# Optimization experiments

Hardware: AMD Instinct MI355X
Metric: run time of the kernel (lower is better)

Reference implementation:

```python
import jax, jax.numpy as jnp
import numpy as np

NEG_INF = -1e9  # fp32-safe mask value for non-edges
ALPHA = 0.2     # LeakyReLU negative slope


def setup_inputs() -> dict:
    key = jax.random.key(0)
    k1, k2, k3, k4, k5 = jax.random.split(key, 5)
    N, F_in, H, F_out = 4096, 512, 8, 64
    features = jax.random.normal(k1, (N, F_in), dtype=jnp.float32)
    adjacency_matrix = jax.random.randint(k2, (N, N), 0, 2, dtype=jnp.int32)
    W = jax.random.normal(k3, (H, F_in, F_out), dtype=jnp.float32) * (F_in ** -0.5)
    a_src = jax.random.normal(k4, (H, F_out), dtype=jnp.float32) * (F_out ** -0.5)
    a_dst = jax.random.normal(k5, (H, F_out), dtype=jnp.float32) * (F_out ** -0.5)
    return {"features": features, "adjacency_matrix": adjacency_matrix,
            "W": W, "a_src": a_src, "a_dst": a_dst}


def reference(features, adjacency_matrix, W, a_src, a_dst):
    # Per-head linear projection: [H, N, F_out]
    Wh = jnp.einsum('nf,hfo->hno', features, W)
    # Attention logits e_ij = LeakyReLU(a_src . Wh_i + a_dst . Wh_j)
    src = jnp.einsum('hno,ho->hn', Wh, a_src)  # [H, N]
    dst = jnp.einsum('hno,ho->hn', Wh, a_dst)  # [H, N]
    e = jax.nn.leaky_relu(src[:, :, None] + dst[:, None, :], ALPHA)  # [H, N, N]
    mask = (adjacency_matrix > 0)[None, :, :]
    e = jnp.where(mask, e, jnp.asarray(NEG_INF, e.dtype))
    attn = jax.nn.softmax(e, axis=-1)  # adjacency-masked row softmax
    h = jnp.einsum('hij,hjo->hio', attn, Wh)  # [H, N, F_out]
    h = jax.nn.elu(h)
    # concat=True: torch.cat over feature dim -> [N, H*F_out]
    return jnp.transpose(h, (1, 0, 2)).reshape(h.shape[1], -1)
```

## Files before the change

### kernel.cpp

```cpp
#include <hip/hip_runtime.h>
#include <hip/hip_bf16.h>

typedef __bf16 bf16x8 __attribute__((ext_vector_type(8)));
typedef _Float16 f16x8 __attribute__((ext_vector_type(8)));
typedef _Float16 f16x2 __attribute__((ext_vector_type(2)));
typedef float  f32x4  __attribute__((ext_vector_type(4)));
typedef unsigned short u16x8 __attribute__((ext_vector_type(8)));
typedef unsigned short us4   __attribute__((ext_vector_type(4)));

#define HH    8
#define NN    4096
#define FIN   512
#define FOUT  64
#define ALPHA 0.2f

__global__ __launch_bounds__(256) void k_transpose_w(
    const float* __restrict__ Wsrc, __hip_bfloat16* __restrict__ WT) {
    __shared__ __hip_bfloat16 lt[64][65];
    const int h  = blockIdx.x >> 3;
    const int f0 = (blockIdx.x & 7) * 64;
    const int tid = threadIdx.x;
#pragma unroll
    for (int p = 0; p < 16; ++p) {
        int f = p * 4 + (tid >> 6);
        int o = tid & 63;
        lt[f][o] = __float2bfloat16(Wsrc[((size_t)h * FIN + f0 + f) * FOUT + o]);
    }
    __syncthreads();
#pragma unroll
    for (int p = 0; p < 16; ++p) {
        int o = p * 4 + (tid >> 6);
        int f = tid & 63;
        WT[((size_t)h * FOUT + o) * FIN + f0 + f] = lt[f][o];
    }
}

__global__ __launch_bounds__(256) void k_prep(
    int* __restrict__ adj,
    const float* __restrict__ feat,
    const __hip_bfloat16* __restrict__ WT,
    const float* __restrict__ a_src,
    const float* __restrict__ a_dst,
    unsigned short* __restrict__ WhT,
    float* __restrict__ srcv,
    unsigned short* __restrict__ Ebf, unsigned short* __restrict__ Fbf) {
    __shared__ alignas(16) __hip_bfloat16 lfeat[32][520];

    const int tid = threadIdx.x;

    if (blockIdx.x < 2048) {
        const size_t base = (size_t)blockIdx.x * 8192;
        unsigned m = 0;
#pragma unroll
        for (int p = 0; p < 8; ++p) {
            int4 v = *(const int4*)(adj + base + tid * 32 + p * 4);
            m |= (unsigned)(v.x > 0) << (p * 4);
            m |= (unsigned)(v.y > 0) << (p * 4 + 1);
            m |= (unsigned)(v.z > 0) << (p * 4 + 2);
            m |= (unsigned)(v.w > 0) << (p * 4 + 3);
        }
        __syncthreads();
        ((unsigned*)adj)[base + tid] = m;
        return;
    }

    const int pb   = blockIdx.x - 2048;
    const int tile = pb & 127;
    const int hgy  = pb >> 7;

#pragma unroll
    for (int p = 0; p < 16; ++p) {
        int idx  = p * 256 + tid;
        int row  = idx >> 7;
        int col4 = (idx & 127) * 4;
        float4 f = *(const float4*)(feat + (size_t)(tile * 32 + row) * FIN + col4);
        __hip_bfloat16* dst = &lfeat[row][col4];
        dst[0] = __float2bfloat16(f.x); dst[1] = __float2bfloat16(f.y);
        dst[2] = __float2bfloat16(f.z); dst[3] = __float2bfloat16(f.w);
    }
    __syncthreads();

    const int h     = hgy * 4 + (tid >> 6);
    const int lane  = tid & 63;
    const int row16 = lane & 15;
    const int quad  = lane >> 4;

    const unsigned short* WTu = (const unsigned short*)WT + (size_t)h * FOUT * FIN;

    f32x4 acc[2][4] = {};
    for (int k0 = 0; k0 < FIN; k0 += 32) {
        bf16x8 a0 = *(const bf16x8*)&lfeat[row16][k0 + quad * 8];
        bf16x8 a1 = *(const bf16x8*)&lfeat[16 + row16][k0 + quad * 8];
#pragma unroll
        for (int ot = 0; ot < 4; ++ot) {
            bf16x8 b = *(const bf16x8*)(WTu + (size_t)(ot * 16 + row16) * FIN + k0 + quad * 8);
            acc[0][ot] = __builtin_amdgcn_mfma_f32_16x16x32_bf16(a0, b, acc[0][ot], 0, 0, 0);
            acc[1][ot] = __builtin_amdgcn_mfma_f32_16x16x32_bf16(a1, b, acc[1][ot], 0, 0, 0);
        }
    }

#pragma unroll
    for (int g = 0; g < 2; ++g)
#pragma unroll
        for (int ot = 0; ot < 4; ++ot) {
            us4 u;
#pragma unroll
            for (int r = 0; r < 4; ++r)
                u[r] = __builtin_bit_cast(unsigned short, (_Float16)acc[g][ot][r]);
            *(us4*)(WhT + (size_t)(h * FOUT + ot * 16 + row16) * NN
                        + tile * 32 + g * 16 + quad * 4) = u;
        }

    float asv[4], adv[4];
#pragma unroll
    for (int ot = 0; ot < 4; ++ot) {
        asv[ot] = a_src[h * FOUT + ot * 16 + row16];
        adv[ot] = a_dst[h * FOUT + ot * 16 + row16];
    }
#pragma unroll
    for (int g = 0; g < 2; ++g)
#pragma unroll
        for (int r = 0; r < 4; ++r) {
            float ss = 0.f, dd = 0.f;
#pragma unroll
            for (int ot = 0; ot < 4; ++ot) {
                ss += acc[g][ot][r] * asv[ot];
                dd += acc[g][ot][r] * adv[ot];
            }
            ss += __shfl_xor(ss, 1); ss += __shfl_xor(ss, 2);
            ss += __shfl_xor(ss, 4); ss += __shfl_xor(ss, 8);
            dd += __shfl_xor(dd, 1); dd += __shfl_xor(dd, 2);
            dd += __shfl_xor(dd, 4); dd += __shfl_xor(dd, 8);
            if (row16 == 0) {
                int n = tile * 32 + g * 16 + quad * 4 + r;
                srcv[h * NN + n] = ss;
                _Float16 e = (_Float16)__expf(dd);
                _Float16 f = (_Float16)__expf(ALPHA * dd);
                Ebf[h * NN + n] = __builtin_bit_cast(unsigned short, e);
                Fbf[h * NN + n] = __builtin_bit_cast(unsigned short, f);
            }
        }
}

__global__ __launch_bounds__(512, 4) void k_flash(
    const unsigned* __restrict__ maskp,
    const float* __restrict__ srcv,
    const unsigned short* __restrict__ Ebf,
    const unsigned short* __restrict__ Fbf,
    const unsigned short* __restrict__ WhT,
    float* __restrict__ out) {
    __shared__ float st[2][64 * 68];
    __shared__ float lds_l[2][64];

    unsigned* lmask = (unsigned*)&st[0][0];

    const int tid   = threadIdx.x;
    const int seg   = tid >> 6;
    const int lane  = tid & 63;
    const int row16 = lane & 15;
    const int quad  = lane >> 4;
    const int shl   = quad * 8;
    const int tile  = blockIdx.x;
    const int h     = blockIdx.y;

#pragma unroll
    for (int p = 0; p < 4; ++p) {
        int tt = tid + p * 512;
        int c  = tt >> 6;
        int o  = (tt & 63) * 16;
        int4 v = *(const int4*)((const char*)maskp
                                + (size_t)(tile * 32 + c) * 32768 + o);
        int row = c * 2 + (o >> 9);
        int dw  = (o & 511) >> 2;
        *(int4*)&lmask[row * 132 + dw] = v;
    }
    __syncthreads();

    f16x2 Es2[4], Fs2[4];
#pragma unroll
    for (int g = 0; g < 4; ++g) {
        float si = srcv[h * NN + tile * 64 + g * 16 + row16];
        _Float16 e = (_Float16)__expf(si);
        _Float16 f = (_Float16)__expf(ALPHA * si);
        Es2[g][0] = e; Es2[g][1] = e;
        Fs2[g][0] = f; Fs2[g][1] = f;
    }
    const int mbase = row16 * 132 + seg * 16;

    const unsigned short* Eb = Ebf + h * NN + seg * 512;
    const unsigned short* Fb = Fbf + h * NN + seg * 512;
    const unsigned short* wh = WhT + (size_t)h * FOUT * NN + seg * 512;

    f32x4 acc[4][4] = {};
    float lsum[4]   = {};
    const f16x2 ones2 = {(_Float16)1.0f, (_Float16)1.0f};

    int t = (seg * 2) & 15;

#pragma unroll 1
    for (int i = 0; i < 16; ++i) {
        const int jj = t * 32 + shl;
        union { f16x8 v8; f16x2 h2[4]; } evu, fvu;
        evu.v8 = *(const f16x8*)(Eb + jj);
        fvu.v8 = *(const f16x8*)(Fb + jj);
        f16x8 b[4];
#pragma unroll
        for (int ot = 0; ot < 4; ++ot)
            b[ot] = *(const f16x8*)(wh + (size_t)(ot * 16 + row16) * NN + jj);

#pragma unroll
        for (int g = 0; g < 4; ++g) {
            unsigned mb = lmask[mbase + g * 2112 + t] >> shl;
            union { f16x8 v8; unsigned w[4]; } au;
#pragma unroll
            for (int kk = 0; kk < 4; ++kk) {
                f16x2 t0 = evu.h2[kk] * Es2[g];
                f16x2 t1 = fvu.h2[kk] * Fs2[g];
                f16x2 p2 = __builtin_elementwise_max(t0, t1);
                unsigned lo = (unsigned)__builtin_amdgcn_sbfe((int)mb, 2 * kk, 1);
                unsigned hi = (unsigned)__builtin_amdgcn_sbfe((int)mb, 2 * kk + 1, 1);
                unsigned w  = (lo & 0xFFFFu) | (hi & 0xFFFF0000u);
                unsigned pw = __builtin_bit_cast(unsigned, p2) & w;
                f16x2 mp2   = __builtin_bit_cast(f16x2, pw);
                au.w[kk] = pw;
#if __has_builtin(__builtin_amdgcn_fdot2)
                lsum[g] = __builtin_amdgcn_fdot2(mp2, ones2, lsum[g], false);
#else
                lsum[g] += (float)mp2[0] + (float)mp2[1];
#endif
            }
            __builtin_amdgcn_s_setprio(1);
#pragma unroll
            for (int ot = 0; ot < 4; ++ot)
                acc[g][ot] = __builtin_amdgcn_mfma_f32_16x16x32_f16(au.v8, b[ot], acc[g][ot], 0, 0, 0);
            __builtin_amdgcn_s_setprio(0);
        }
        t = (t + 1) & 15;
    }

#pragma unroll
    for (int g = 0; g < 4; ++g) {
        lsum[g] += __shfl_xor(lsum[g], 16);
        lsum[g] += __shfl_xor(lsum[g], 32);
    }

    __syncthreads();

    auto stash = [&](int buf) {
#pragma unroll
        for (int g = 0; g < 4; ++g)
#pragma unroll
            for (int ot = 0; ot < 4; ++ot)
#pragma unroll
                for (int r = 0; r < 4; ++r)
                    st[buf][(g * 16 + quad * 4 + r) * 68 + ot * 16 + row16] = acc[g][ot][r];
        if (quad == 0)
#pragma unroll
            for (int g = 0; g < 4; ++g)
                lds_l[buf][g * 16 + row16] = lsum[g];
    };
    auto addin = [&](int buf) {
#pragma unroll
        for (int g = 0; g < 4; ++g) {
#pragma unroll
            for (int ot = 0; ot < 4; ++ot)
#pragma unroll
                for (int r = 0; r < 4; ++r)
                    acc[g][ot][r] += st[buf][(g * 16 + quad * 4 + r) * 68 + ot * 16 + row16];
            lsum[g] += lds_l[buf][g * 16 + row16];
        }
    };

    if (seg == 1) stash(0);
    if (seg == 3) stash(1);
    __syncthreads();
    if (seg == 0) addin(0);
    if (seg == 2) addin(1);
    __syncthreads();
    if (seg == 5) stash(0);
    if (seg == 7) stash(1);
    __syncthreads();
    if (seg == 4) addin(0);
    if (seg == 6) addin(1);
    __syncthreads();
    if (seg == 2) stash(0);
    if (seg == 6) stash(1);
    __syncthreads();
    if (seg == 0) addin(0);
    if (seg == 4) addin(1);
    __syncthreads();
    if (seg == 4) stash(0);
    __syncthreads();
    if (seg == 0) {
        addin(0);
#pragma unroll
        for (int g = 0; g < 4; ++g)
#pragma unroll
            for (int r = 0; r < 4; ++r) {
                int   qr  = quad * 4 + r;
                float l   = __shfl(lsum[g], qr);
                float rl  = 1.0f / l;
#pragma unroll
                for (int ot = 0; ot < 4; ++ot) {
                    float v = acc[g][ot][r] * rl;
                    float y = v > 0.f ? v : __expf(v) - 1.f;
                    st[0][(g * 16 + qr) * 68 + ot * 16 + row16] = y;
                }
            }
    }
    __syncthreads();
#pragma unroll
    for (int p = 0; p < 2; ++p) {
        int f    = tid + p * 512;
        int row  = f >> 4;
        int col4 = (f & 15) * 4;
        float4 v = *(const float4*)&st[0][row * 68 + col4];
        *(float4*)&out[(size_t)(tile * 64 + row) * (HH * FOUT) + h * FOUT + col4] = v;
    }
}

extern "C" void kernel_launch(void* const* d_in, const int* in_sizes, int n_in,
                              void* d_out, int out_size, void* d_ws, size_t ws_size,
                              hipStream_t stream) {
    const float* features = (const float*)d_in[0];
    int*         adj      = (int*)d_in[1];
    const float* W        = (const float*)d_in[2];
    const float* a_src    = (const float*)d_in[3];
    const float* a_dst    = (const float*)d_in[4];
    float*       out      = (float*)d_out;

    char* ws = (char*)d_ws;
    __hip_bfloat16* WT   = (__hip_bfloat16*)(ws);
    unsigned short* WhT  = (unsigned short*)(ws + (512 << 10));
    float*          srcv = (float*)(ws + (512 << 10) + (4 << 20));
    unsigned short* Ebf  = (unsigned short*)(ws + (512 << 10) + (4 << 20) + (128 << 10));
    unsigned short* Fbf  = (unsigned short*)(ws + (512 << 10) + (4 << 20) + (192 << 10));

    k_transpose_w<<<dim3(64), 256, 0, stream>>>(W, WT);
    k_prep<<<dim3(2048 + 256), 256, 0, stream>>>(adj, features, WT, a_src, a_dst,
                                                 WhT, srcv, Ebf, Fbf);
    k_flash<<<dim3(64, 8), 512, 0, stream>>>((const unsigned*)adj, srcv, Ebf, Fbf,
                                             WhT, out);
}
```

Baseline: 167.5 us.

## Halve flash block size, software-prefetch next tile, and store bitmask in workspace

Measured after the change: 164.5 us. Within noise of the previous version (-1.8%).

```diff
diff --git a/kernel.cpp b/kernel.cpp
--- a/kernel.cpp
+++ b/kernel.cpp
@@ -36,7 +36,8 @@
 }
 
 __global__ __launch_bounds__(256) void k_prep(
-    int* __restrict__ adj,
+    const int* __restrict__ adj,
+    unsigned* __restrict__ maskdst, int mstride,
     const float* __restrict__ feat,
     const __hip_bfloat16* __restrict__ WT,
     const float* __restrict__ a_src,
@@ -60,7 +61,7 @@
             m |= (unsigned)(v.w > 0) << (p * 4 + 3);
         }
         __syncthreads();
-        ((unsigned*)adj)[base + tid] = m;
+        maskdst[(size_t)blockIdx.x * mstride + tid] = m;
         return;
     }
 
@@ -142,8 +143,8 @@
         }
 }
 
-__global__ __launch_bounds__(512, 4) void k_flash(
-    const unsigned* __restrict__ maskp,
+__global__ __launch_bounds__(256, 3) void k_flash(
+    const unsigned* __restrict__ maskp, int mstride,
     const float* __restrict__ srcv,
     const unsigned short* __restrict__ Ebf,
     const unsigned short* __restrict__ Fbf,
@@ -164,12 +165,12 @@
     const int h     = blockIdx.y;
 
 #pragma unroll
-    for (int p = 0; p < 4; ++p) {
-        int tt = tid + p * 512;
+    for (int p = 0; p < 8; ++p) {
+        int tt = tid + p * 256;
         int c  = tt >> 6;
         int o  = (tt & 63) * 16;
         int4 v = *(const int4*)((const char*)maskp
-                                + (size_t)(tile * 32 + c) * 32768 + o);
+                                + ((size_t)(tile * 32 + c) * mstride) * 4 + o);
         int row = c * 2 + (o >> 9);
         int dw  = (o & 511) >> 2;
         *(int4*)&lmask[row * 132 + dw] = v;
@@ -185,32 +186,51 @@
         Es2[g][0] = e; Es2[g][1] = e;
         Fs2[g][0] = f; Fs2[g][1] = f;
     }
-    const int mbase = row16 * 132 + seg * 16;
-
-    const unsigned short* Eb = Ebf + h * NN + seg * 512;
-    const unsigned short* Fb = Fbf + h * NN + seg * 512;
-    const unsigned short* wh = WhT + (size_t)h * FOUT * NN + seg * 512;
+    const int mbase = row16 * 132 + seg * 32;
+
+    const unsigned short* Eb = Ebf + h * NN + seg * 1024;
+    const unsigned short* Fb = Fbf + h * NN + seg * 1024;
+    const unsigned short* wh = WhT + (size_t)h * FOUT * NN + seg * 1024;
 
     f32x4 acc[4][4] = {};
     float lsum[4]   = {};
     const f16x2 ones2 = {(_Float16)1.0f, (_Float16)1.0f};
 
-    int t = (seg * 2) & 15;
-
-#pragma unroll 1
-    for (int i = 0; i < 16; ++i) {
+    int t = (seg * 8) & 31;
+    union { f16x8 v8; f16x2 h2[4]; } evu, fvu;
+    f16x8 bc[4];
+    unsigned mc[4];
+    {
         const int jj = t * 32 + shl;
-        union { f16x8 v8; f16x2 h2[4]; } evu, fvu;
         evu.v8 = *(const f16x8*)(Eb + jj);
         fvu.v8 = *(const f16x8*)(Fb + jj);
-        f16x8 b[4];
 #pragma unroll
         for (int ot = 0; ot < 4; ++ot)
-            b[ot] = *(const f16x8*)(wh + (size_t)(ot * 16 + row16) * NN + jj);
+            bc[ot] = *(const f16x8*)(wh + (size_t)(ot * 16 + row16) * NN + jj);
+#pragma unroll
+        for (int g = 0; g < 4; ++g)
+            mc[g] = lmask[mbase + g * 2112 + t];
+    }
+
+#pragma unroll 1
+    for (int i = 0; i < 32; ++i) {
+        const int tn = (t + 1) & 31;
+        const int jn = tn * 32 + shl;
+        union { f16x8 v8; f16x2 h2[4]; } evn, fvn;
+        evn.v8 = *(const f16x8*)(Eb + jn);
+        fvn.v8 = *(const f16x8*)(Fb + jn);
+        f16x8 bn[4];
+#pragma unroll
+        for (int ot = 0; ot < 4; ++ot)
+            bn[ot] = *(const f16x8*)(wh + (size_t)(ot * 16 + row16) * NN + jn);
+        unsigned mn[4];
+#pragma unroll
+        for (int g = 0; g < 4; ++g)
+            mn[g] = lmask[mbase + g * 2112 + tn];
 
 #pragma unroll
         for (int g = 0; g < 4; ++g) {
-            unsigned mb = lmask[mbase + g * 2112 + t] >> shl;
+            unsigned mb = mc[g] >> shl;
             union { f16x8 v8; unsigned w[4]; } au;
 #pragma unroll
             for (int kk = 0; kk < 4; ++kk) {
@@ -232,10 +252,16 @@
             __builtin_amdgcn_s_setprio(1);
 #pragma unroll
             for (int ot = 0; ot < 4; ++ot)
-                acc[g][ot] = __builtin_amdgcn_mfma_f32_16x16x32_f16(au.v8, b[ot], acc[g][ot], 0, 0, 0);
+                acc[g][ot] = __builtin_amdgcn_mfma_f32_16x16x32_f16(au.v8, bc[ot], acc[g][ot], 0, 0, 0);
             __builtin_amdgcn_s_setprio(0);
         }
-        t = (t + 1) & 15;
+        evu.v8 = evn.v8;
+        fvu.v8 = fvn.v8;
+#pragma unroll
+        for (int ot = 0; ot < 4; ++ot) bc[ot] = bn[ot];
+#pragma unroll
+        for (int g = 0; g < 4; ++g) mc[g] = mn[g];
+        t = tn;
     }
 
 #pragma unroll
@@ -277,19 +303,7 @@
     if (seg == 0) addin(0);
     if (seg == 2) addin(1);
     __syncthreads();
-    if (seg == 5) stash(0);
-    if (seg == 7) stash(1);
-    __syncthreads();
-    if (seg == 4) addin(0);
-    if (seg == 6) addin(1);
-    __syncthreads();
     if (seg == 2) stash(0);
-    if (seg == 6) stash(1);
-    __syncthreads();
-    if (seg == 0) addin(0);
-    if (seg == 4) addin(1);
-    __syncthreads();
-    if (seg == 4) stash(0);
     __syncthreads();
     if (seg == 0) {
         addin(0);
@@ -310,8 +324,8 @@
     }
     __syncthreads();
 #pragma unroll
-    for (int p = 0; p < 2; ++p) {
-        int f    = tid + p * 512;
+    for (int p = 0; p < 4; ++p) {
+        int f    = tid + p * 256;
         int row  = f >> 4;
         int col4 = (f & 15) * 4;
         float4 v = *(const float4*)&st[0][row * 68 + col4];
@@ -336,9 +350,20 @@
     unsigned short* Ebf  = (unsigned short*)(ws + (512 << 10) + (4 << 20) + (128 << 10));
     unsigned short* Fbf  = (unsigned short*)(ws + (512 << 10) + (4 << 20) + (192 << 10));
 
+    const size_t mask_off = (512 << 10) + (4 << 20) + (256 << 10);
+    unsigned* maskp; int mstride;
+    if (ws_size >= mask_off + (2u << 20)) {
+        maskp   = (unsigned*)(ws + mask_off);
+        mstride = 256;
+    } else {
+        maskp   = (unsigned*)adj;
+        mstride = 8192;
+    }
+
     k_transpose_w<<<dim3(64), 256, 0, stream>>>(W, WT);
-    k_prep<<<dim3(2048 + 256), 256, 0, stream>>>(adj, features, WT, a_src, a_dst,
+    k_prep<<<dim3(2048 + 256), 256, 0, stream>>>(adj, maskp, mstride,
+                                                 features, WT, a_src, a_dst,
                                                  WhT, srcv, Ebf, Fbf);
-    k_flash<<<dim3(64, 8), 512, 0, stream>>>((const unsigned*)adj, srcv, Ebf, Fbf,
+    k_flash<<<dim3(64, 8), 256, 0, stream>>>(maskp, mstride, srcv, Ebf, Fbf,
                                              WhT, out);
 }
```
